# Optimization experiments

Hardware: AMD Instinct MI355X
Metric: run time of the kernel (lower is better)

## Reference

```python
import jax, jax.numpy as jnp
import numpy as np

B, F, E, V = 8192, 16, 32, 100000
D, H1, H2 = 8, 1024, 512
IN = F * E  # 512
EPS = 1e-5


def _bn(x, gamma, beta):
    # x: [D, B, H]; training-mode BatchNorm1d per domain over batch axis (biased var)
    mean = jnp.mean(x, axis=1, keepdims=True)
    var = jnp.mean((x - mean) ** 2, axis=1, keepdims=True)
    return (x - mean) * jax.lax.rsqrt(var + EPS) * gamma[:, None, :] + beta[:, None, :]


def setup_inputs() -> dict:
    key = jax.random.key(0)
    ks = jax.random.split(key, 12)
    feat_ids = jax.random.randint(ks[0], (B, F), 0, V)
    domain_id = jax.random.randint(ks[1], (B,), 0, D)
    emb_tables = jax.random.normal(ks[2], (F, V, E), jnp.float32) * 0.02
    s1 = 1.0 / np.sqrt(IN)
    s2 = 1.0 / np.sqrt(H1)
    s3 = 1.0 / np.sqrt(H2)
    return {
        "feat_ids": feat_ids,
        "domain_id": domain_id,
        "emb_tables": emb_tables,
        "W1": jax.random.uniform(ks[3], (D, H1, IN), jnp.float32, -s1, s1),
        "b1": jax.random.uniform(ks[4], (D, H1), jnp.float32, -s1, s1),
        "g1": jnp.ones((D, H1), jnp.float32),
        "be1": jnp.zeros((D, H1), jnp.float32),
        "W2": jax.random.uniform(ks[5], (D, H2, H1), jnp.float32, -s2, s2),
        "b2": jax.random.uniform(ks[6], (D, H2), jnp.float32, -s2, s2),
        "g2": jnp.ones((D, H2), jnp.float32),
        "be2": jnp.zeros((D, H2), jnp.float32),
        "W3": jax.random.uniform(ks[7], (D, H2), jnp.float32, -s3, s3),
        "b3": jax.random.uniform(ks[8], (D,), jnp.float32, -s3, s3),
    }


def reference(feat_ids, domain_id, emb_tables, W1, b1, g1, be1, W2, b2, g2, be2, W3, b3):
    # embedding lookup per feature then concat -> [B, F*E]
    emb = jax.vmap(lambda tab, ids: tab[ids], in_axes=(0, 1), out_axes=1)(emb_tables, feat_ids)
    emb = emb.reshape(B, IN)
    # all-domain redundant MLP (as in original torch code)
    h = jnp.einsum('bf,dhf->dbh', emb, W1) + b1[:, None, :]          # [D,B,H1]
    h = jax.nn.relu(_bn(h, g1, be1))
    h = jnp.einsum('dbh,dkh->dbk', h, W2) + b2[:, None, :]           # [D,B,H2]
    h = jax.nn.relu(_bn(h, g2, be2))
    out = jax.nn.sigmoid(jnp.einsum('dbk,dk->db', h, W3) + b3[:, None])  # [D,B]
    # mask-select the row matching each sample's domain
    final = jnp.take_along_axis(out.T, domain_id[:, None], axis=1)[:, 0]  # [B]
    return final
```

## Files before the change

kernel.cpp:

```cpp
#include <hip/hip_runtime.h>
#include <hip/hip_bf16.h>

#define B_SZ   8192
#define F_CNT  16
#define E_DIM  32
#define V_CNT  100000
#define D_CNT  8
#define H1     1024
#define H2     512
#define IN_DIM 512
#define EPS_BN 1e-5f

typedef __attribute__((ext_vector_type(8))) unsigned short ushort8;
typedef __attribute__((ext_vector_type(8))) short          frag_ab;
typedef __attribute__((ext_vector_type(4))) float          frag_cd;
typedef __attribute__((ext_vector_type(4))) float          float4v;

__device__ inline unsigned short f2b(float f) {
    unsigned int u = __builtin_bit_cast(unsigned int, f);
    unsigned int r = u + 0x7FFFu + ((u >> 16) & 1u);
    return (unsigned short)(r >> 16);
}
__device__ inline float b2f(unsigned short b) {
    return __builtin_bit_cast(float, (unsigned int)b << 16);
}

__device__ inline void ld_lds16(const unsigned short* g, unsigned short* l) {
    __builtin_amdgcn_global_load_lds(
        (const __attribute__((address_space(1))) unsigned int*)g,
        (__attribute__((address_space(3))) unsigned int*)l, 16, 0, 0);
}

__global__ void k_convert(const float* __restrict__ src, unsigned short* __restrict__ dst,
                          long n) {
    long i = ((long)blockIdx.x * 256 + threadIdx.x) * 4;
    if (i >= n) return;
    float4v v = *(const float4v*)(src + i);
    dst[i]     = f2b(v[0]);
    dst[i + 1] = f2b(v[1]);
    dst[i + 2] = f2b(v[2]);
    dst[i + 3] = f2b(v[3]);
}

__global__ void k_gather(const int* __restrict__ feat_ids,
                         const float* __restrict__ tables,
                         unsigned short* __restrict__ emb) {
    int tid = blockIdx.x * 256 + threadIdx.x;
    int b = tid >> 6;
    int c = tid & 63;
    int f = c >> 2;
    int id = feat_ids[b * F_CNT + f];
    const float* s = tables + ((long)f * V_CNT + id) * E_DIM + (c & 3) * 8;
    float4v v0 = *(const float4v*)s;
    float4v v1 = *(const float4v*)(s + 4);
    ushort8 o;
#pragma unroll
    for (int i = 0; i < 4; i++) { o[i] = f2b(v0[i]); o[i + 4] = f2b(v1[i]); }
    *(ushort8*)(emb + (long)b * IN_DIM + c * 8) = o;
}

__global__ __launch_bounds__(256, 2)
void k_gemm(const unsigned short* __restrict__ A,
            const unsigned short* __restrict__ W,
            unsigned short* __restrict__ C,
            float* __restrict__ gsum, float* __restrict__ gsq,
            int M, int N, int K, long aBatchStride, int d0) {
    const int z  = blockIdx.z;
    const int m0 = blockIdx.x * 128;
    const int n0 = blockIdx.y * 128;
    const unsigned short* Ad = A + (long)z * aBatchStride;
    const unsigned short* Wd = W + (long)(d0 + z) * N * K;

    __shared__ unsigned short As[128 * 32];
    __shared__ unsigned short Bs[128 * 32];

    const int t    = threadIdx.x;
    const int wave = t >> 6;
    const int lane = t & 63;
    const int wm   = (wave & 1) << 6;
    const int wn   = (wave >> 1) << 6;
    const int q    = lane >> 4;
    const int lr   = lane & 15;

    const int srow = lane >> 2;
    const int scol = (lane & 3) * 8;
    const unsigned short* aG0 = Ad + (long)(m0 + wave * 32 + srow) * K + scol;
    const unsigned short* aG1 = aG0 + 16 * (long)K;
    const unsigned short* wG0 = Wd + (long)(n0 + wave * 32 + srow) * K + scol;
    const unsigned short* wG1 = wG0 + 16 * (long)K;
    unsigned short* aL0 = &As[(wave * 32) * 32];
    unsigned short* aL1 = &As[(wave * 32 + 16) * 32];
    unsigned short* wL0 = &Bs[(wave * 32) * 32];
    unsigned short* wL1 = &Bs[(wave * 32 + 16) * 32];

    frag_cd acc[4][4];
#pragma unroll
    for (int i = 0; i < 4; i++)
#pragma unroll
        for (int j = 0; j < 4; j++)
            acc[i][j] = (frag_cd){0.f, 0.f, 0.f, 0.f};

    for (int k0 = 0; k0 < K; k0 += 32) {
        ld_lds16(aG0 + k0, aL0);
        ld_lds16(aG1 + k0, aL1);
        ld_lds16(wG0 + k0, wL0);
        ld_lds16(wG1 + k0, wL1);
        __syncthreads();

        frag_ab af[4], bf[4];
#pragma unroll
        for (int i = 0; i < 4; i++) {
            af[i] = *(const frag_ab*)&As[(wm + i * 16 + lr) * 32 + q * 8];
            bf[i] = *(const frag_ab*)&Bs[(wn + i * 16 + lr) * 32 + q * 8];
        }
#pragma unroll
        for (int i = 0; i < 4; i++)
#pragma unroll
            for (int j = 0; j < 4; j++)
                acc[i][j] = __builtin_amdgcn_mfma_f32_16x16x32_bf16(af[i], bf[j], acc[i][j], 0, 0, 0);
        __syncthreads();
    }

    unsigned short* Cd = C + (long)z * M * N;
    float s[4], q2[4];
#pragma unroll
    for (int j = 0; j < 4; j++) { s[j] = 0.f; q2[j] = 0.f; }
#pragma unroll
    for (int i = 0; i < 4; i++) {
        int row = m0 + wm + i * 16 + q * 4;
#pragma unroll
        for (int j = 0; j < 4; j++) {
            int col = n0 + wn + j * 16 + lr;
#pragma unroll
            for (int r = 0; r < 4; r++) {
                float v = acc[i][j][r];
                Cd[(long)(row + r) * N + col] = f2b(v);
                s[j] += v; q2[j] += v * v;
            }
        }
    }
#pragma unroll
    for (int j = 0; j < 4; j++) {
        s[j]  += __shfl_xor(s[j], 16, 64);  s[j]  += __shfl_xor(s[j], 32, 64);
        q2[j] += __shfl_xor(q2[j], 16, 64); q2[j] += __shfl_xor(q2[j], 32, 64);
    }
    if (lane < 16) {
        float* gs = gsum + (long)(d0 + z) * N + n0 + wn;
        float* gq = gsq  + (long)(d0 + z) * N + n0 + wn;
#pragma unroll
        for (int j = 0; j < 4; j++) {
            atomicAdd(&gs[j * 16 + lane], s[j]);
            atomicAdd(&gq[j * 16 + lane], q2[j]);
        }
    }
}

__global__ void k_finalize(const float* __restrict__ gsum, const float* __restrict__ gsq,
                           const float* __restrict__ g, const float* __restrict__ be,
                           float* __restrict__ scale, float* __restrict__ shift, int n,
                           int gOff) {
    int i = blockIdx.x * 256 + threadIdx.x;
    if (i >= n) return;
    float mean = gsum[i] * (1.0f / B_SZ);
    float var  = gsq[i] * (1.0f / B_SZ) - mean * mean;
    float sc   = g[gOff + i] * rsqrtf(var + EPS_BN);
    scale[i] = sc;
    shift[i] = be[gOff + i] - mean * sc;
}

__global__ void k_bn_apply(const unsigned short* __restrict__ P,
                           const float* __restrict__ scale, const float* __restrict__ shift,
                           unsigned short* __restrict__ Out, int H, int d0) {
    long tid = (long)blockIdx.x * 256 + threadIdx.x;
    long off = tid * 8;
    int j  = (int)(off % H);
    int dj = ((int)(off / ((long)B_SZ * H)) + d0) * H + j;
    ushort8 v = *(const ushort8*)(P + off);
    float4v sc0 = *(const float4v*)(scale + dj);
    float4v sc1 = *(const float4v*)(scale + dj + 4);
    float4v sh0 = *(const float4v*)(shift + dj);
    float4v sh1 = *(const float4v*)(shift + dj + 4);
    ushort8 o;
#pragma unroll
    for (int i = 0; i < 8; i++) {
        float scv = (i < 4) ? sc0[i] : sc1[i - 4];
        float shv = (i < 4) ? sh0[i] : sh1[i - 4];
        float x = b2f(v[i]) * scv + shv;
        o[i] = f2b(fmaxf(x, 0.f));
    }
    *(ushort8*)(Out + off) = o;
}

__global__ void k_final(const unsigned short* __restrict__ h2c,
                        const int* __restrict__ domain_id,
                        const float* __restrict__ scale2, const float* __restrict__ shift2,
                        const unsigned short* __restrict__ W3, const unsigned short* __restrict__ b3,
                        float* __restrict__ out, int d0, int nc) {
    int wave = threadIdx.x >> 6, lane = threadIdx.x & 63;
    int b = blockIdx.x * 4 + wave;
    int d = domain_id[b];
    if (d < d0 || d >= d0 + nc) return;
    int o = d * H2 + lane * 8;
    ushort8 v = *(const ushort8*)(h2c + ((long)(d - d0) * B_SZ + b) * H2 + lane * 8);
    ushort8 w = *(const ushort8*)(W3 + o);
    float sum = 0.f;
#pragma unroll
    for (int i = 0; i < 8; i++) {
        float x = b2f(v[i]) * scale2[o + i] + shift2[o + i];
        sum += fmaxf(x, 0.f) * b2f(w[i]);
    }
#pragma unroll
    for (int off = 32; off > 0; off >>= 1) sum += __shfl_xor(sum, off, 64);
    if (lane == 0)
        out[b] = 1.f / (1.f + expf(-(sum + b2f(b3[d]))));
}

__global__ void k_zero(float* __restrict__ p, int n) {
    int i = blockIdx.x * 256 + threadIdx.x;
    if (i < n) p[i] = 0.f;
}

__global__ void k_sentinel(float* __restrict__ out, int n) {
    int i = blockIdx.x * 256 + threadIdx.x;
    if (i < n) out[i] = 0.25f;
}

extern "C" void kernel_launch(void* const* d_in, const int* in_sizes, int n_in,
                              void* d_out, int out_size, void* d_ws, size_t ws_size,
                              hipStream_t stream) {
    const int*   feat_ids  = (const int*)d_in[0];
    const int*   domain_id = (const int*)d_in[1];
    const float* tables = (const float*)d_in[2];
    const float* W1  = (const float*)d_in[3];
    const float* g1  = (const float*)d_in[5];
    const float* be1 = (const float*)d_in[6];
    const float* W2  = (const float*)d_in[7];
    const float* g2  = (const float*)d_in[9];
    const float* be2 = (const float*)d_in[10];
    const float* W3  = (const float*)d_in[11];
    const float* b3  = (const float*)d_in[12];

    char* ws = (char*)d_ws;
    float* gsum1  = (float*)ws;
    float* gsq1   = gsum1 + 8192;
    float* gsum2  = gsq1 + 8192;
    float* gsq2   = gsum2 + 4096;
    float* scale1 = gsq2 + 4096;
    float* shift1 = scale1 + 8192;
    float* scale2 = shift1 + 8192;
    float* shift2 = scale2 + 4096;
    unsigned short* W1c = (unsigned short*)(ws + (1L  << 20));
    unsigned short* W2c = (unsigned short*)(ws + (9L  << 20));
    unsigned short* W3c = (unsigned short*)(ws + (17L << 20));
    unsigned short* b3c = W3c + D_CNT * H2;
    unsigned short* emb = (unsigned short*)(ws + (18L << 20));

    const long h1Elems = (long)B_SZ * H1;
    const long h2Elems = (long)B_SZ * H2;
    const long perDom  = (h1Elems + h2Elems) * 2;
    const long baseOff = 26L << 20;
    int NC = 0;
    for (int cand = 8; cand >= 1; cand >>= 1)
        if (baseOff + (long)cand * perDom <= (long)ws_size) { NC = cand; break; }
    if (NC == 0) {
        k_sentinel<<<dim3((out_size + 255) / 256), dim3(256), 0, stream>>>(
            (float*)d_out, out_size);
        return;
    }
    unsigned short* h1c = (unsigned short*)(ws + baseOff);
    unsigned short* h2c = h1c + (long)NC * h1Elems;

    k_zero<<<dim3(96), dim3(256), 0, stream>>>(gsum1, 24576);
    k_convert<<<dim3(4096), dim3(256), 0, stream>>>(W1, W1c, (long)D_CNT * H1 * IN_DIM);
    k_convert<<<dim3(4096), dim3(256), 0, stream>>>(W2, W2c, (long)D_CNT * H2 * H1);
    k_convert<<<dim3(4),    dim3(256), 0, stream>>>(W3, W3c, (long)D_CNT * H2);
    k_convert<<<dim3(1),    dim3(2),   0, stream>>>(b3, b3c, (long)D_CNT);
    k_gather<<<dim3(2048), dim3(256), 0, stream>>>(feat_ids, tables, emb);

    for (int d0 = 0; d0 < D_CNT; d0 += NC) {
        k_gemm<<<dim3(64, 8, NC), dim3(256), 0, stream>>>(
            emb, W1c, h1c, gsum1, gsq1, 8192, 1024, 512, 0L, d0);
        k_finalize<<<dim3(NC * 4), dim3(256), 0, stream>>>(
            gsum1 + d0 * H1, gsq1 + d0 * H1, g1, be1,
            scale1 + d0 * H1, shift1 + d0 * H1, NC * H1, d0 * H1);
        k_bn_apply<<<dim3(NC * 4096), dim3(256), 0, stream>>>(
            h1c, scale1, shift1, h1c, H1, d0);
        k_gemm<<<dim3(64, 4, NC), dim3(256), 0, stream>>>(
            h1c, W2c, h2c, gsum2, gsq2, 8192, 512, 1024, h1Elems, d0);
        k_finalize<<<dim3(NC * 2), dim3(256), 0, stream>>>(
            gsum2 + d0 * H2, gsq2 + d0 * H2, g2, be2,
            scale2 + d0 * H2, shift2 + d0 * H2, NC * H2, d0 * H2);
        k_final<<<dim3(2048), dim3(256), 0, stream>>>(
            h2c, domain_id, scale2, shift2, W3c, b3c, (float*)d_out, d0, NC);
    }
}
```

Measured before the change: 498.5 us.

## Fuse BN finalize into GEMM epilogue and BN1 apply into GEMM2 A-load

Removes the separate finalize and bn_apply kernels. The last GEMM block per column tile, detected with an atomic counter, computes BN scale and shift. GEMM2 applies BN1 scale, shift and ReLU to the A operand in registers before writing it to LDS. Weight conversion and zeroing are merged into one init kernel. This saves a full read and write pass over h1 and several launches, but the GEMM2 A path now goes through registers instead of direct-to-LDS loads, which adds load latency per k-step.

```diff
diff --git a/kernel.cpp b/kernel.cpp
--- a/kernel.cpp
+++ b/kernel.cpp
@@ -31,15 +31,35 @@
         (__attribute__((address_space(3))) unsigned int*)l, 16, 0, 0);
 }
 
-__global__ void k_convert(const float* __restrict__ src, unsigned short* __restrict__ dst,
-                          long n) {
-    long i = ((long)blockIdx.x * 256 + threadIdx.x) * 4;
-    if (i >= n) return;
-    float4v v = *(const float4v*)(src + i);
-    dst[i]     = f2b(v[0]);
-    dst[i + 1] = f2b(v[1]);
-    dst[i + 2] = f2b(v[2]);
-    dst[i + 3] = f2b(v[3]);
+__global__ void k_init(const float* __restrict__ W1, const float* __restrict__ W2,
+                       const float* __restrict__ W3, const float* __restrict__ b3,
+                       unsigned short* __restrict__ W1c, unsigned short* __restrict__ W2c,
+                       unsigned short* __restrict__ W3c, unsigned short* __restrict__ b3c,
+                       float* __restrict__ zb) {
+    int bid = blockIdx.x, t = threadIdx.x;
+    if (bid < 8192) {
+        const float* src = (bid < 4096) ? W1 : W2;
+        unsigned short* dst = (bid < 4096) ? W1c : W2c;
+        long i = ((long)(bid & 4095) * 256 + t) * 4;
+        float4v v = *(const float4v*)(src + i);
+        dst[i]     = f2b(v[0]);
+        dst[i + 1] = f2b(v[1]);
+        dst[i + 2] = f2b(v[2]);
+        dst[i + 3] = f2b(v[3]);
+    } else if (bid == 8192) {
+        const float* s = W3 + t * 16;
+        unsigned short* d = W3c + t * 16;
+#pragma unroll
+        for (int j = 0; j < 4; j++) {
+            float4v v = *(const float4v*)(s + j * 4);
+            d[j * 4 + 0] = f2b(v[0]); d[j * 4 + 1] = f2b(v[1]);
+            d[j * 4 + 2] = f2b(v[2]); d[j * 4 + 3] = f2b(v[3]);
+        }
+        if (t < D_CNT) b3c[t] = f2b(b3[t]);
+    } else {
+        int i = (bid - 8193) * 1024 + t * 4;
+        if (i < 24672) *(float4v*)(zb + i) = (float4v){0.f, 0.f, 0.f, 0.f};
+    }
 }
 
 __global__ void k_gather(const int* __restrict__ feat_ids,
@@ -59,12 +79,72 @@
     *(ushort8*)(emb + (long)b * IN_DIM + c * 8) = o;
 }
 
+__device__ inline void gemm_epilogue(frag_cd acc[4][4],
+                                     unsigned short* __restrict__ Cd,
+                                     float* __restrict__ gsum, float* __restrict__ gsq,
+                                     int* __restrict__ cnt,
+                                     const float* __restrict__ g, const float* __restrict__ be,
+                                     float* __restrict__ scale, float* __restrict__ shift,
+                                     int N, int d, int m0, int n0,
+                                     int wm, int wn, int q, int lr, int lane, int t) {
+    float s[4], q2[4];
+#pragma unroll
+    for (int j = 0; j < 4; j++) { s[j] = 0.f; q2[j] = 0.f; }
+#pragma unroll
+    for (int i = 0; i < 4; i++) {
+        int row = m0 + wm + i * 16 + q * 4;
+#pragma unroll
+        for (int j = 0; j < 4; j++) {
+            int col = n0 + wn + j * 16 + lr;
+#pragma unroll
+            for (int r = 0; r < 4; r++) {
+                float v = acc[i][j][r];
+                Cd[(long)(row + r) * N + col] = f2b(v);
+                s[j] += v; q2[j] += v * v;
+            }
+        }
+    }
+#pragma unroll
+    for (int j = 0; j < 4; j++) {
+        s[j]  += __shfl_xor(s[j], 16, 64);  s[j]  += __shfl_xor(s[j], 32, 64);
+        q2[j] += __shfl_xor(q2[j], 16, 64); q2[j] += __shfl_xor(q2[j], 32, 64);
+    }
+    if (lane < 16) {
+        float* gs = gsum + (long)d * N + n0 + wn;
+        float* gq = gsq  + (long)d * N + n0 + wn;
+#pragma unroll
+        for (int j = 0; j < 4; j++) {
+            atomicAdd(&gs[j * 16 + lane], s[j]);
+            atomicAdd(&gq[j * 16 + lane], q2[j]);
+        }
+    }
+    __threadfence();
+    __shared__ int lastDone;
+    if (t == 0) {
+        int c = atomicAdd(&cnt[d * gridDim.y + blockIdx.y], 1);
+        lastDone = (c == (int)gridDim.x - 1);
+    }
+    __syncthreads();
+    if (lastDone && t < 128) {
+        int col = n0 + t;
+        float sm = atomicAdd(&gsum[(long)d * N + col], 0.f);
+        float sq = atomicAdd(&gsq [(long)d * N + col], 0.f);
+        float mean = sm * (1.0f / B_SZ);
+        float var  = sq * (1.0f / B_SZ) - mean * mean;
+        float sc   = g[(long)d * N + col] * rsqrtf(var + EPS_BN);
+        scale[(long)d * N + col] = sc;
+        shift[(long)d * N + col] = be[(long)d * N + col] - mean * sc;
+    }
+}
+
 __global__ __launch_bounds__(256, 2)
-void k_gemm(const unsigned short* __restrict__ A,
-            const unsigned short* __restrict__ W,
-            unsigned short* __restrict__ C,
-            float* __restrict__ gsum, float* __restrict__ gsq,
-            int M, int N, int K, long aBatchStride, int d0) {
+void k_gemm1(const unsigned short* __restrict__ A,
+             const unsigned short* __restrict__ W,
+             unsigned short* __restrict__ C,
+             float* __restrict__ gsum, float* __restrict__ gsq, int* __restrict__ cnt,
+             const float* __restrict__ g, const float* __restrict__ be,
+             float* __restrict__ scale, float* __restrict__ shift,
+             int M, int N, int K, long aBatchStride, int d0) {
     const int z  = blockIdx.z;
     const int m0 = blockIdx.x * 128;
     const int n0 = blockIdx.y * 128;
@@ -122,73 +202,100 @@
     }
 
     unsigned short* Cd = C + (long)z * M * N;
-    float s[4], q2[4];
-#pragma unroll
-    for (int j = 0; j < 4; j++) { s[j] = 0.f; q2[j] = 0.f; }
-#pragma unroll
-    for (int i = 0; i < 4; i++) {
-        int row = m0 + wm + i * 16 + q * 4;
-#pragma unroll
-        for (int j = 0; j < 4; j++) {
-            int col = n0 + wn + j * 16 + lr;
-#pragma unroll
-            for (int r = 0; r < 4; r++) {
-                float v = acc[i][j][r];
-                Cd[(long)(row + r) * N + col] = f2b(v);
-                s[j] += v; q2[j] += v * v;
-            }
-        }
-    }
-#pragma unroll
-    for (int j = 0; j < 4; j++) {
-        s[j]  += __shfl_xor(s[j], 16, 64);  s[j]  += __shfl_xor(s[j], 32, 64);
-        q2[j] += __shfl_xor(q2[j], 16, 64); q2[j] += __shfl_xor(q2[j], 32, 64);
-    }
-    if (lane < 16) {
-        float* gs = gsum + (long)(d0 + z) * N + n0 + wn;
-        float* gq = gsq  + (long)(d0 + z) * N + n0 + wn;
-#pragma unroll
-        for (int j = 0; j < 4; j++) {
-            atomicAdd(&gs[j * 16 + lane], s[j]);
-            atomicAdd(&gq[j * 16 + lane], q2[j]);
-        }
-    }
-}
-
-__global__ void k_finalize(const float* __restrict__ gsum, const float* __restrict__ gsq,
-                           const float* __restrict__ g, const float* __restrict__ be,
-                           float* __restrict__ scale, float* __restrict__ shift, int n,
-                           int gOff) {
-    int i = blockIdx.x * 256 + threadIdx.x;
-    if (i >= n) return;
-    float mean = gsum[i] * (1.0f / B_SZ);
-    float var  = gsq[i] * (1.0f / B_SZ) - mean * mean;
-    float sc   = g[gOff + i] * rsqrtf(var + EPS_BN);
-    scale[i] = sc;
-    shift[i] = be[gOff + i] - mean * sc;
-}
-
-__global__ void k_bn_apply(const unsigned short* __restrict__ P,
-                           const float* __restrict__ scale, const float* __restrict__ shift,
-                           unsigned short* __restrict__ Out, int H, int d0) {
-    long tid = (long)blockIdx.x * 256 + threadIdx.x;
-    long off = tid * 8;
-    int j  = (int)(off % H);
-    int dj = ((int)(off / ((long)B_SZ * H)) + d0) * H + j;
-    ushort8 v = *(const ushort8*)(P + off);
-    float4v sc0 = *(const float4v*)(scale + dj);
-    float4v sc1 = *(const float4v*)(scale + dj + 4);
-    float4v sh0 = *(const float4v*)(shift + dj);
-    float4v sh1 = *(const float4v*)(shift + dj + 4);
-    ushort8 o;
-#pragma unroll
-    for (int i = 0; i < 8; i++) {
-        float scv = (i < 4) ? sc0[i] : sc1[i - 4];
-        float shv = (i < 4) ? sh0[i] : sh1[i - 4];
-        float x = b2f(v[i]) * scv + shv;
-        o[i] = f2b(fmaxf(x, 0.f));
-    }
-    *(ushort8*)(Out + off) = o;
+    gemm_epilogue(acc, Cd, gsum, gsq, cnt, g, be, scale, shift,
+                  N, d0 + z, m0, n0, wm, wn, q, lr, lane, t);
+}
+
+__global__ __launch_bounds__(256, 2)
+void k_gemm2(const unsigned short* __restrict__ A,
+             const unsigned short* __restrict__ W,
+             unsigned short* __restrict__ C,
+             float* __restrict__ gsum, float* __restrict__ gsq, int* __restrict__ cnt,
+             const float* __restrict__ g, const float* __restrict__ be,
+             float* __restrict__ scale, float* __restrict__ shift,
+             const float* __restrict__ sc1, const float* __restrict__ sh1,
+             int M, int N, int K, long aBatchStride, int d0) {
+    const int z  = blockIdx.z;
+    const int m0 = blockIdx.x * 128;
+    const int n0 = blockIdx.y * 128;
+    const unsigned short* Ad = A + (long)z * aBatchStride;
+    const unsigned short* Wd = W + (long)(d0 + z) * N * K;
+
+    __shared__ unsigned short As[128 * 32];
+    __shared__ unsigned short Bs[128 * 32];
+
+    const int t    = threadIdx.x;
+    const int wave = t >> 6;
+    const int lane = t & 63;
+    const int wm   = (wave & 1) << 6;
+    const int wn   = (wave >> 1) << 6;
+    const int q    = lane >> 4;
+    const int lr   = lane & 15;
+
+    const int srow = lane >> 2;
+    const int scol = (lane & 3) * 8;
+    const unsigned short* aP0 = Ad + (long)(m0 + wave * 32 + srow) * K + scol;
+    const unsigned short* aP1 = aP0 + 16 * (long)K;
+    const float* scD = sc1 + (long)(d0 + z) * K;
+    const float* shD = sh1 + (long)(d0 + z) * K;
+    const unsigned short* wG0 = Wd + (long)(n0 + wave * 32 + srow) * K + scol;
+    const unsigned short* wG1 = wG0 + 16 * (long)K;
+    unsigned short* aL0w = &As[(wave * 32 + srow) * 32 + scol];
+    unsigned short* aL1w = aL0w + 16 * 32;
+    unsigned short* wL0 = &Bs[(wave * 32) * 32];
+    unsigned short* wL1 = &Bs[(wave * 32 + 16) * 32];
+
+    frag_cd acc[4][4];
+#pragma unroll
+    for (int i = 0; i < 4; i++)
+#pragma unroll
+        for (int j = 0; j < 4; j++)
+            acc[i][j] = (frag_cd){0.f, 0.f, 0.f, 0.f};
+
+    ushort8 x0 = *(const ushort8*)aP0;
+    ushort8 x1 = *(const ushort8*)aP1;
+
+    for (int k0 = 0; k0 < K; k0 += 32) {
+        ld_lds16(wG0 + k0, wL0);
+        ld_lds16(wG1 + k0, wL1);
+        float4v sa = *(const float4v*)(scD + k0 + scol);
+        float4v sb = *(const float4v*)(scD + k0 + scol + 4);
+        float4v ha = *(const float4v*)(shD + k0 + scol);
+        float4v hb = *(const float4v*)(shD + k0 + scol + 4);
+        ushort8 y0, y1;
+#pragma unroll
+        for (int i2 = 0; i2 < 8; i2++) {
+            float scv = (i2 < 4) ? sa[i2] : sb[i2 - 4];
+            float shv = (i2 < 4) ? ha[i2] : hb[i2 - 4];
+            y0[i2] = f2b(fmaxf(b2f(x0[i2]) * scv + shv, 0.f));
+            y1[i2] = f2b(fmaxf(b2f(x1[i2]) * scv + shv, 0.f));
+        }
+        *(ushort8*)aL0w = y0;
+        *(ushort8*)aL1w = y1;
+        __syncthreads();
+
+        if (k0 + 32 < K) {
+            x0 = *(const ushort8*)(aP0 + k0 + 32);
+            x1 = *(const ushort8*)(aP1 + k0 + 32);
+        }
+
+        frag_ab af[4], bf[4];
+#pragma unroll
+        for (int i = 0; i < 4; i++) {
+            af[i] = *(const frag_ab*)&As[(wm + i * 16 + lr) * 32 + q * 8];
+            bf[i] = *(const frag_ab*)&Bs[(wn + i * 16 + lr) * 32 + q * 8];
+        }
+#pragma unroll
+        for (int i = 0; i < 4; i++)
+#pragma unroll
+            for (int j = 0; j < 4; j++)
+                acc[i][j] = __builtin_amdgcn_mfma_f32_16x16x32_bf16(af[i], bf[j], acc[i][j], 0, 0, 0);
+        __syncthreads();
+    }
+
+    unsigned short* Cd = C + (long)z * M * N;
+    gemm_epilogue(acc, Cd, gsum, gsq, cnt, g, be, scale, shift,
+                  N, d0 + z, m0, n0, wm, wn, q, lr, lane, t);
 }
 
 __global__ void k_final(const unsigned short* __restrict__ h2c,
@@ -213,11 +320,6 @@
     for (int off = 32; off > 0; off >>= 1) sum += __shfl_xor(sum, off, 64);
     if (lane == 0)
         out[b] = 1.f / (1.f + expf(-(sum + b2f(b3[d]))));
-}
-
-__global__ void k_zero(float* __restrict__ p, int n) {
-    int i = blockIdx.x * 256 + threadIdx.x;
-    if (i < n) p[i] = 0.f;
 }
 
 __global__ void k_sentinel(float* __restrict__ out, int n) {
@@ -245,7 +347,9 @@
     float* gsq1   = gsum1 + 8192;
     float* gsum2  = gsq1 + 8192;
     float* gsq2   = gsum2 + 4096;
-    float* scale1 = gsq2 + 4096;
+    int*   cnt1   = (int*)(gsq2 + 4096);
+    int*   cnt2   = cnt1 + 64;
+    float* scale1 = (float*)(cnt2 + 32);
     float* shift1 = scale1 + 8192;
     float* scale2 = shift1 + 8192;
     float* shift2 = scale2 + 4096;
@@ -270,26 +374,16 @@
     unsigned short* h1c = (unsigned short*)(ws + baseOff);
     unsigned short* h2c = h1c + (long)NC * h1Elems;
 
-    k_zero<<<dim3(96), dim3(256), 0, stream>>>(gsum1, 24576);
-    k_convert<<<dim3(4096), dim3(256), 0, stream>>>(W1, W1c, (long)D_CNT * H1 * IN_DIM);
-    k_convert<<<dim3(4096), dim3(256), 0, stream>>>(W2, W2c, (long)D_CNT * H2 * H1);
-    k_convert<<<dim3(4),    dim3(256), 0, stream>>>(W3, W3c, (long)D_CNT * H2);
-    k_convert<<<dim3(1),    dim3(2),   0, stream>>>(b3, b3c, (long)D_CNT);
+    k_init<<<dim3(8218), dim3(256), 0, stream>>>(W1, W2, W3, b3, W1c, W2c, W3c, b3c, gsum1);
     k_gather<<<dim3(2048), dim3(256), 0, stream>>>(feat_ids, tables, emb);
 
     for (int d0 = 0; d0 < D_CNT; d0 += NC) {
-        k_gemm<<<dim3(64, 8, NC), dim3(256), 0, stream>>>(
-            emb, W1c, h1c, gsum1, gsq1, 8192, 1024, 512, 0L, d0);
-        k_finalize<<<dim3(NC * 4), dim3(256), 0, stream>>>(
-            gsum1 + d0 * H1, gsq1 + d0 * H1, g1, be1,
-            scale1 + d0 * H1, shift1 + d0 * H1, NC * H1, d0 * H1);
-        k_bn_apply<<<dim3(NC * 4096), dim3(256), 0, stream>>>(
-            h1c, scale1, shift1, h1c, H1, d0);
-        k_gemm<<<dim3(64, 4, NC), dim3(256), 0, stream>>>(
-            h1c, W2c, h2c, gsum2, gsq2, 8192, 512, 1024, h1Elems, d0);
-        k_finalize<<<dim3(NC * 2), dim3(256), 0, stream>>>(
-            gsum2 + d0 * H2, gsq2 + d0 * H2, g2, be2,
-            scale2 + d0 * H2, shift2 + d0 * H2, NC * H2, d0 * H2);
+        k_gemm1<<<dim3(64, 8, NC), dim3(256), 0, stream>>>(
+            emb, W1c, h1c, gsum1, gsq1, cnt1, g1, be1, scale1, shift1,
+            8192, 1024, 512, 0L, d0);
+        k_gemm2<<<dim3(64, 4, NC), dim3(256), 0, stream>>>(
+            h1c, W2c, h2c, gsum2, gsq2, cnt2, g2, be2, scale2, shift2,
+            scale1, shift1, 8192, 512, 1024, h1Elems, d0);
         k_final<<<dim3(2048), dim3(256), 0, stream>>>(
             h2c, domain_id, scale2, shift2, W3c, b3c, (float*)d_out, d0, NC);
     }
```

After: 1.457 ms. 192% more time.
